# Optimization experiments

Hardware: AMD Instinct MI355X
Metric: run time of the kernel (lower is better)

Reference implementation:

```python
import jax, jax.numpy as jnp
import numpy as np

B, S, D = 2, 2048, 1024
H = 16
HD = D // H  # 64

def setup_inputs() -> dict:
    key = jax.random.key(0)
    ks = jax.random.split(key, 6)
    scale = 0.02
    return {
        "query": jax.random.normal(ks[0], (B, S, D), dtype=jnp.float32),
        "key":   jax.random.normal(ks[1], (B, S, D), dtype=jnp.float32),
        "value": jax.random.normal(ks[2], (B, S, D), dtype=jnp.float32),
        "Wq": jax.random.normal(ks[3], (D, D), dtype=jnp.float32) * scale,
        "bq": jnp.zeros((D,), dtype=jnp.float32),
        "Wk": jax.random.normal(ks[4], (D, D), dtype=jnp.float32) * scale,
        "bk": jnp.zeros((D,), dtype=jnp.float32),
        "Wv": jax.random.normal(ks[5], (D, D), dtype=jnp.float32) * scale,
        "bv": jnp.zeros((D,), dtype=jnp.float32),
    }

def reference(query, key, value, Wq, bq, Wk, bk, Wv, bv):
    b, s, d = query.shape
    # Linear projections (weights stored as (in, out))
    q = query @ Wq + bq   # [B,S,D]
    k = key   @ Wk + bk
    v = value @ Wv + bv
    # split heads -> [B,H,S,HD]
    q = q.reshape(b, s, H, HD).transpose(0, 2, 1, 3)
    k = k.reshape(b, s, H, HD).transpose(0, 2, 1, 3)
    v = v.reshape(b, s, H, HD).transpose(0, 2, 1, 3)
    # scaled dot-product attention (no mask; dropout = identity in eval)
    scores = jnp.einsum("bhqd,bhkd->bhqk", q, k) / jnp.sqrt(jnp.float32(HD))
    attn = jax.nn.softmax(scores, axis=-1)
    out = jnp.einsum("bhqk,bhkd->bhqd", attn, v)
    # merge heads -> [B,S,D]
    return out.transpose(0, 2, 1, 3).reshape(b, s, d)
```

## Files before the change

### kernel.cpp

```cpp
#include <hip/hip_runtime.h>
#include <stdint.h>

#define D_  1024
#define S_  2048
#define B_  2
#define H_  16
#define HD_ 64
#define M_  (B_*S_)
#define KVB 64

typedef unsigned short u16;
typedef __attribute__((ext_vector_type(8)))  __bf16 bf16x8;
typedef __attribute__((ext_vector_type(4)))  float  f32x4;
typedef __attribute__((ext_vector_type(16))) float  f32x16;

__device__ __forceinline__ u16 f2bf(float f) {
    __bf16 h = (__bf16)f;
    union { __bf16 h; u16 u; } x; x.h = h;
    return x.u;
}

__device__ __forceinline__ void gload_lds16(const void* g, void* l) {
    __builtin_amdgcn_global_load_lds(
        (const __attribute__((address_space(1))) uint32_t*)g,
        (__attribute__((address_space(3))) uint32_t*)l, 16, 0, 0);
}

__global__ __launch_bounds__(256) void prep_kernel(
    const float* __restrict__ q, const float* __restrict__ k, const float* __restrict__ v,
    u16* __restrict__ Xq, u16* __restrict__ Xk, u16* __restrict__ Xv,
    const float* __restrict__ Wq, const float* __restrict__ Wk, const float* __restrict__ Wv,
    u16* __restrict__ Wtq, u16* __restrict__ Wtk, u16* __restrict__ Wtv)
{
    __shared__ u16 t[64][65];
    int bid = blockIdx.x;
    if (bid < 12288) {
        int sl = bid >> 12;
        int bx = bid & 4095;
        const float* in = sl == 0 ? q : (sl == 1 ? k : v);
        u16* out = sl == 0 ? Xq : (sl == 1 ? Xk : Xv);
        int i = (bx * 256 + threadIdx.x) * 4;
        float4 vv = *(const float4*)(in + i);
        ushort4 o;
        o.x = f2bf(vv.x); o.y = f2bf(vv.y); o.z = f2bf(vv.z); o.w = f2bf(vv.w);
        *(ushort4*)(out + i) = o;
    } else {
        int tt = bid - 12288;
        int z = tt >> 8;
        int rem = tt & 255;
        const float* W = z == 0 ? Wq : (z == 1 ? Wk : Wv);
        u16* Wt = z == 0 ? Wtq : (z == 1 ? Wtk : Wtv);
        int k0 = (rem & 15) * 64, n0 = (rem >> 4) * 64;
        int tid = threadIdx.x;
        int c4 = (tid & 15) * 4, r = tid >> 4;
#pragma unroll
        for (int i = 0; i < 4; i++) {
            int row = r + i * 16;
            float4 vv = *(const float4*)(W + (uint64_t)(k0 + row) * D_ + n0 + c4);
            t[row][c4 + 0] = f2bf(vv.x);
            t[row][c4 + 1] = f2bf(vv.y);
            t[row][c4 + 2] = f2bf(vv.z);
            t[row][c4 + 3] = f2bf(vv.w);
        }
        __syncthreads();
#pragma unroll
        for (int i = 0; i < 4; i++) {
            int nrow = r + i * 16;
            ushort4 o;
            o.x = t[c4 + 0][nrow]; o.y = t[c4 + 1][nrow];
            o.z = t[c4 + 2][nrow]; o.w = t[c4 + 3][nrow];
            *(ushort4*)(Wt + (uint64_t)(n0 + nrow) * D_ + k0 + c4) = o;
        }
    }
}

__global__ __launch_bounds__(256) void gemm_qkv(
    const u16* __restrict__ Xq, const u16* __restrict__ Xk, const u16* __restrict__ Xv,
    const u16* __restrict__ Wtq, const u16* __restrict__ Wtk, const u16* __restrict__ Wtv,
    const float* __restrict__ bq, const float* __restrict__ bk, const float* __restrict__ bv,
    u16* __restrict__ Qo, u16* __restrict__ Ko, u16* __restrict__ Vo)
{
    int p = blockIdx.z;
    const u16* X    = p == 0 ? Xq  : (p == 1 ? Xk  : Xv);
    const u16* Wt   = p == 0 ? Wtq : (p == 1 ? Wtk : Wtv);
    const float* bias = p == 0 ? bq : (p == 1 ? bk : bv);
    u16* out = p == 0 ? Qo : (p == 1 ? Ko : Vo);
    float scale = p == 0 ? 0.125f : 1.0f;

    __shared__ __align__(16) u16 As[3][64 * 32];
    __shared__ __align__(16) u16 Bs[3][128 * 32];

    int tid = threadIdx.x;
    int lane = tid & 63, wid = tid >> 6;
    int lrow = lane & 15, lk = lane >> 4;
    int wr = wid >> 1, wc = wid & 1;
    int bm = blockIdx.x, bn = blockIdx.y;

    f32x4 acc[2][4] = {};

    const uint64_t Xrow0 = (uint64_t)bm * 64 * D_;
    const uint64_t Wrow0 = (uint64_t)bn * 128 * D_;

    auto stage = [&](int buf, int kt) {
        int k0 = kt * 32;
        {
            int row = tid >> 2;
            int cg = (tid & 3) ^ ((row >> 1) & 3);
            gload_lds16(X + Xrow0 + (uint64_t)row * D_ + k0 + cg * 8,
                        (char*)As[buf] + wid * 1024);
        }
#pragma unroll
        for (int it = 0; it < 2; ++it) {
            int i = it * 256 + tid;
            int row = i >> 2;
            int cg = (i & 3) ^ ((row >> 1) & 3);
            gload_lds16(Wt + Wrow0 + (uint64_t)row * D_ + k0 + cg * 8,
                        (char*)Bs[buf] + it * 4096 + wid * 1024);
        }
    };

    stage(0, 0);
    stage(1, 1);
    asm volatile("s_waitcnt vmcnt(3)" ::: "memory");
    __builtin_amdgcn_s_barrier();

    const int NKT = D_ / 32;
    for (int kt = 0; kt < NKT; ++kt) {
        int cur = kt % 3;
        if (kt + 2 < NKT) stage((kt + 2) % 3, kt + 2);

        bf16x8 a[2], b[4];
#pragma unroll
        for (int m = 0; m < 2; m++) {
            int r = wr * 32 + m * 16 + lrow;
            a[m] = *(const bf16x8*)((const char*)As[cur] + r * 64 + ((lk ^ ((r >> 1) & 3)) * 16));
        }
#pragma unroll
        for (int n = 0; n < 4; n++) {
            int r = wc * 64 + n * 16 + lrow;
            b[n] = *(const bf16x8*)((const char*)Bs[cur] + r * 64 + ((lk ^ ((r >> 1) & 3)) * 16));
        }
        if (p < 2) {
#pragma unroll
            for (int m = 0; m < 2; m++)
#pragma unroll
                for (int n = 0; n < 4; n++)
                    acc[m][n] = __builtin_amdgcn_mfma_f32_16x16x32_bf16(a[m], b[n], acc[m][n], 0, 0, 0);
        } else {
#pragma unroll
            for (int m = 0; m < 2; m++)
#pragma unroll
                for (int n = 0; n < 4; n++)
                    acc[m][n] = __builtin_amdgcn_mfma_f32_16x16x32_bf16(b[n], a[m], acc[m][n], 0, 0, 0);
        }

        if (kt + 1 < NKT) {
            if (kt + 2 < NKT)
                asm volatile("s_waitcnt vmcnt(3)" ::: "memory");
            else
                asm volatile("s_waitcnt vmcnt(0)" ::: "memory");
            __builtin_amdgcn_s_barrier();
        }
    }

    if (p < 2) {
#pragma unroll
        for (int m = 0; m < 2; m++) {
            int grow_base = bm * 64 + wr * 32 + m * 16 + lk * 4;
#pragma unroll
            for (int n = 0; n < 4; n++) {
                int gcol = bn * 128 + wc * 64 + n * 16 + lrow;
                float bb = bias[gcol];
                int h = gcol >> 6, hd = gcol & 63;
#pragma unroll
                for (int j = 0; j < 4; j++) {
                    int grow = grow_base + j;
                    int b_ = grow >> 11, s = grow & 2047;
                    out[(((uint64_t)(b_ * H_ + h)) * S_ + s) * HD_ + hd] =
                        f2bf((acc[m][n][j] + bb) * scale);
                }
            }
        }
    } else {
#pragma unroll
        for (int m = 0; m < 2; m++) {
            int sg = bm * 64 + wr * 32 + m * 16 + lrow;
            int b_ = sg >> 11, s = sg & 2047;
#pragma unroll
            for (int n = 0; n < 4; n++) {
                int ch_base = bn * 128 + wc * 64 + n * 16 + lk * 4;
#pragma unroll
                for (int j = 0; j < 4; j++) {
                    int ch = ch_base + j;
                    int h = ch >> 6, hd = ch & 63;
                    out[(((uint64_t)(b_ * H_ + h)) * HD_ + hd) * S_ + s] =
                        f2bf(acc[m][n][j] + bias[ch]);
                }
            }
        }
    }
}

__global__ __launch_bounds__(256) void attn_kernel(
    const u16* __restrict__ Q, const u16* __restrict__ K,
    const u16* __restrict__ VT, float* __restrict__ out)
{
    __shared__ __align__(16) char smem[32768];

    int lin = blockIdx.x;
    int swz = (lin & 7) * 64 + (lin >> 3);
    int qt = swz & 15, bh = swz >> 4;

    int tid = threadIdx.x;
    int w = tid >> 6, lane = tid & 63;
    int q5 = lane & 31, h = lane >> 5;

    bf16x8 qf[4];
    const u16* Qrow = Q + ((uint64_t)bh * S_ + qt * 128 + w * 32 + q5) * HD_;
#pragma unroll
    for (int kk = 0; kk < 4; kk++)
        qf[kk] = *(const bf16x8*)(Qrow + kk * 16 + h * 8);

    f32x16 o_acc[2] = {};
    float m_run = -1e30f, l_run = 0.f;

    const char* Kbase = (const char*)(K  + (uint64_t)bh * S_ * HD_);
    const char* Vbase = (const char*)(VT + (uint64_t)bh * HD_ * S_);

    auto stage = [&](int buf, int t) {
        int kv0 = t * KVB;
#pragma unroll
        for (int it = 0; it < 2; ++it) {
            int i = it * 256 + tid;
            int o = i * 16;
            int rr = o >> 7;
            int os = o ^ ((rr & 7) << 4);
            gload_lds16(Kbase + (uint64_t)kv0 * 128 + os,
                        smem + buf * 8192 + it * 4096 + w * 1024);
            gload_lds16(Vbase + (uint64_t)rr * (S_ * 2) + kv0 * 2 + (os & 127),
                        smem + 16384 + buf * 8192 + it * 4096 + w * 1024);
        }
    };

    stage(0, 0);
    __syncthreads();
    int cur = 0;

    const int NT = S_ / KVB;
    for (int t = 0; t < NT; ++t) {
        if (t + 1 < NT) stage(cur ^ 1, t + 1);

        const char* Kc = smem + cur * 8192;
        const char* Vc = smem + 16384 + cur * 8192;
        int sw = (q5 & 7) << 4;

        f32x16 sacc[2] = {};
        __builtin_amdgcn_s_setprio(1);
#pragma unroll
        for (int c = 0; c < 2; c++) {
            int rb = (c * 32 + q5) * 128;
#pragma unroll
            for (int kk = 0; kk < 4; kk++) {
                bf16x8 kf = *(const bf16x8*)(Kc + rb + ((kk * 32 + h * 16) ^ sw));
                sacc[c] = __builtin_amdgcn_mfma_f32_32x32x16_bf16(kf, qf[kk], sacc[c], 0, 0, 0);
            }
        }
        __builtin_amdgcn_s_setprio(0);

        float mp = sacc[0][0];
#pragma unroll
        for (int r = 1; r < 16; r++) mp = fmaxf(mp, sacc[0][r]);
#pragma unroll
        for (int r = 0; r < 16; r++) mp = fmaxf(mp, sacc[1][r]);
        mp = fmaxf(mp, __shfl_xor(mp, 32, 64));
        float mnew = fmaxf(m_run, mp);
        float sc = __expf(m_run - mnew);
        m_run = mnew;

        float ts = 0.f;
#pragma unroll
        for (int c = 0; c < 2; c++)
#pragma unroll
            for (int r = 0; r < 16; r++) {
                float pv = __expf(sacc[c][r] - mnew);
                sacc[c][r] = pv;
                ts += pv;
            }
        ts += __shfl_xor(ts, 32, 64);
        l_run = l_run * sc + ts;
#pragma unroll
        for (int hb = 0; hb < 2; hb++)
#pragma unroll
            for (int r = 0; r < 16; r++) o_acc[hb][r] *= sc;

        bf16x8 pa[4];
#pragma unroll
        for (int ks = 0; ks < 4; ks++) {
            int c = ks >> 1, gg = ks & 1;
            uint32_t a0, a1, b0, b1;
            asm("v_cvt_pk_bf16_f32 %0, %1, %2" : "=v"(a0) : "v"(sacc[c][8*gg+0]), "v"(sacc[c][8*gg+1]));
            asm("v_cvt_pk_bf16_f32 %0, %1, %2" : "=v"(a1) : "v"(sacc[c][8*gg+2]), "v"(sacc[c][8*gg+3]));
            asm("v_cvt_pk_bf16_f32 %0, %1, %2" : "=v"(b0) : "v"(sacc[c][8*gg+4]), "v"(sacc[c][8*gg+5]));
            asm("v_cvt_pk_bf16_f32 %0, %1, %2" : "=v"(b1) : "v"(sacc[c][8*gg+6]), "v"(sacc[c][8*gg+7]));
            asm volatile("v_permlane32_swap_b32 %0, %1" : "+v"(a0), "+v"(b0));
            asm volatile("v_permlane32_swap_b32 %0, %1" : "+v"(a1), "+v"(b1));
            union { uint32_t u[4]; bf16x8 v; } pu;
            pu.u[0] = a0; pu.u[1] = a1; pu.u[2] = b0; pu.u[3] = b1;
            pa[ks] = pu.v;
        }

        __builtin_amdgcn_s_setprio(1);
#pragma unroll
        for (int hb = 0; hb < 2; hb++) {
            int rb = (hb * 32 + q5) * 128;
#pragma unroll
            for (int ks = 0; ks < 4; ks++) {
                bf16x8 vf = *(const bf16x8*)(Vc + rb + ((ks * 32 + h * 16) ^ sw));
                o_acc[hb] = __builtin_amdgcn_mfma_f32_32x32x16_bf16(vf, pa[ks], o_acc[hb], 0, 0, 0);
            }
        }
        __builtin_amdgcn_s_setprio(0);

        __syncthreads();
        cur ^= 1;
    }

    float inv = 1.0f / l_run;
    int b_ = bh >> 4, head = bh & 15;
    int qq = lane >> 1, c0 = (lane & 1) * 16;
    float* scrw = (float*)smem + w * 1024;
    float* orow = out + ((uint64_t)(b_ * S_ + qt * 128 + w * 32 + qq)) * D_ + head * 64;
#pragma unroll
    for (int hb = 0; hb < 2; hb++) {
#pragma unroll
        for (int r = 0; r < 16; r++) {
            int col = (r & 3) + 8 * (r >> 2) + 4 * h;
            scrw[q5 * 32 + (col ^ ((q5 & 7) << 2))] = o_acc[hb][r] * inv;
        }
        __syncthreads();
#pragma unroll
        for (int j = 0; j < 4; j++) {
            int cb = c0 + j * 4;
            float4 val = *(float4*)&scrw[qq * 32 + (cb ^ ((qq & 7) << 2))];
            *(float4*)(orow + hb * 32 + cb) = val;
        }
        __syncthreads();
    }
}

extern "C" void kernel_launch(void* const* d_in, const int* in_sizes, int n_in,
                              void* d_out, int out_size, void* d_ws, size_t ws_size,
                              hipStream_t stream) {
    const float* q  = (const float*)d_in[0];
    const float* k  = (const float*)d_in[1];
    const float* v  = (const float*)d_in[2];
    const float* Wq = (const float*)d_in[3];
    const float* bq = (const float*)d_in[4];
    const float* Wk = (const float*)d_in[5];
    const float* bk = (const float*)d_in[6];
    const float* Wv = (const float*)d_in[7];
    const float* bv = (const float*)d_in[8];
    float* out = (float*)d_out;

    u16* ws = (u16*)d_ws;
    const size_t XN = (size_t)M_ * D_;
    const size_t WN = (size_t)D_ * D_;
    u16* Xq  = ws;          u16* Xk  = Xq  + XN;  u16* Xv  = Xk  + XN;
    u16* Wtq = Xv + XN;     u16* Wtk = Wtq + WN;  u16* Wtv = Wtk + WN;
    u16* Qb  = Wtv + WN;    u16* Kb  = Qb  + XN;  u16* Vb  = Kb  + XN;

    prep_kernel<<<13056, 256, 0, stream>>>(q, k, v, Xq, Xk, Xv,
                                           Wq, Wk, Wv, Wtq, Wtk, Wtv);
    gemm_qkv<<<dim3(64, 8, 3), 256, 0, stream>>>(Xq, Xk, Xv, Wtq, Wtk, Wtv,
                                                 bq, bk, bv, Qb, Kb, Vb);
    attn_kernel<<<512, 256, 0, stream>>>(Qb, Kb, Vb, out);
}
```

Measured before the change: 219.1 us.

## Use 512-thread attention blocks, exp2 softmax with lazy rescale, tree max

Folds log2(e) into the Q scale so softmax can use exp2 directly. Skips the running-max rescale of the output accumulator unless the new max exceeds the old by more than a threshold. Uses a tree reduction for the row max and split partial sums for the row sum. Attention blocks now hold 8 waves covering 256 queries, so each block does one K/V staging load per thread and the number of blocks is halved. This reduces softmax ALU work and K/V staging traffic per query, at the cost of fewer blocks (256 for 256 CUs), one block's worth of parallelism per CU, and dropping the block-order swizzle that favoured L2 reuse.

```diff
diff --git a/kernel.cpp b/kernel.cpp
--- a/kernel.cpp
+++ b/kernel.cpp
@@ -85,7 +85,7 @@
     const u16* Wt   = p == 0 ? Wtq : (p == 1 ? Wtk : Wtv);
     const float* bias = p == 0 ? bq : (p == 1 ? bk : bv);
     u16* out = p == 0 ? Qo : (p == 1 ? Ko : Vo);
-    float scale = p == 0 ? 0.125f : 1.0f;
+    float scale = p == 0 ? 0.18033688f : 1.0f;
 
     __shared__ __align__(16) u16 As[3][64 * 32];
     __shared__ __align__(16) u16 Bs[3][128 * 32];
@@ -201,22 +201,21 @@
     }
 }
 
-__global__ __launch_bounds__(256) void attn_kernel(
+__global__ __launch_bounds__(512) void attn_kernel(
     const u16* __restrict__ Q, const u16* __restrict__ K,
     const u16* __restrict__ VT, float* __restrict__ out)
 {
     __shared__ __align__(16) char smem[32768];
 
     int lin = blockIdx.x;
-    int swz = (lin & 7) * 64 + (lin >> 3);
-    int qt = swz & 15, bh = swz >> 4;
+    int bh = lin & 31, qt = lin >> 5;
 
     int tid = threadIdx.x;
     int w = tid >> 6, lane = tid & 63;
     int q5 = lane & 31, h = lane >> 5;
 
     bf16x8 qf[4];
-    const u16* Qrow = Q + ((uint64_t)bh * S_ + qt * 128 + w * 32 + q5) * HD_;
+    const u16* Qrow = Q + ((uint64_t)bh * S_ + qt * 256 + w * 32 + q5) * HD_;
 #pragma unroll
     for (int kk = 0; kk < 4; kk++)
         qf[kk] = *(const bf16x8*)(Qrow + kk * 16 + h * 8);
@@ -227,19 +226,16 @@
     const char* Kbase = (const char*)(K  + (uint64_t)bh * S_ * HD_);
     const char* Vbase = (const char*)(VT + (uint64_t)bh * HD_ * S_);
 
+    int o16 = tid * 16;
+    int rr  = o16 >> 7;
+    int os  = o16 ^ ((rr & 7) << 4);
+
     auto stage = [&](int buf, int t) {
         int kv0 = t * KVB;
-#pragma unroll
-        for (int it = 0; it < 2; ++it) {
-            int i = it * 256 + tid;
-            int o = i * 16;
-            int rr = o >> 7;
-            int os = o ^ ((rr & 7) << 4);
-            gload_lds16(Kbase + (uint64_t)kv0 * 128 + os,
-                        smem + buf * 8192 + it * 4096 + w * 1024);
-            gload_lds16(Vbase + (uint64_t)rr * (S_ * 2) + kv0 * 2 + (os & 127),
-                        smem + 16384 + buf * 8192 + it * 4096 + w * 1024);
-        }
+        gload_lds16(Kbase + (uint64_t)kv0 * 128 + os,
+                    smem + buf * 8192 + w * 1024);
+        gload_lds16(Vbase + (uint64_t)rr * (S_ * 2) + kv0 * 2 + (os & 127),
+                    smem + 16384 + buf * 8192 + w * 1024);
     };
 
     stage(0, 0);
@@ -267,31 +263,42 @@
         }
         __builtin_amdgcn_s_setprio(0);
 
-        float mp = sacc[0][0];
-#pragma unroll
-        for (int r = 1; r < 16; r++) mp = fmaxf(mp, sacc[0][r]);
-#pragma unroll
-        for (int r = 0; r < 16; r++) mp = fmaxf(mp, sacc[1][r]);
-        mp = fmaxf(mp, __shfl_xor(mp, 32, 64));
-        float mnew = fmaxf(m_run, mp);
-        float sc = __expf(m_run - mnew);
-        m_run = mnew;
-
-        float ts = 0.f;
+        float tm[16];
+#pragma unroll
+        for (int r = 0; r < 16; r++) tm[r] = fmaxf(sacc[0][r], sacc[1][r]);
+#pragma unroll
+        for (int s2 = 8; s2 > 0; s2 >>= 1)
+#pragma unroll
+            for (int r = 0; r < s2; r++) tm[r] = fmaxf(tm[r], tm[r + s2]);
+        float pmax = fmaxf(tm[0], __shfl_xor(tm[0], 32, 64));
+
+        if (!__all(pmax - m_run <= 8.0f)) {
+            float mnew = fmaxf(m_run, pmax);
+            float sc = __builtin_exp2f(m_run - mnew);
+            m_run = mnew;
+            l_run *= sc;
+#pragma unroll
+            for (int hb = 0; hb < 2; hb++)
+#pragma unroll
+                for (int r = 0; r < 16; r++) o_acc[hb][r] *= sc;
+        }
+
+        float ts0 = 0.f, ts1 = 0.f, ts2 = 0.f, ts3 = 0.f;
 #pragma unroll
         for (int c = 0; c < 2; c++)
 #pragma unroll
-            for (int r = 0; r < 16; r++) {
-                float pv = __expf(sacc[c][r] - mnew);
-                sacc[c][r] = pv;
-                ts += pv;
-            }
+            for (int r = 0; r < 16; r += 4) {
+                float p0 = __builtin_exp2f(sacc[c][r + 0] - m_run);
+                float p1 = __builtin_exp2f(sacc[c][r + 1] - m_run);
+                float p2 = __builtin_exp2f(sacc[c][r + 2] - m_run);
+                float p3 = __builtin_exp2f(sacc[c][r + 3] - m_run);
+                sacc[c][r + 0] = p0; sacc[c][r + 1] = p1;
+                sacc[c][r + 2] = p2; sacc[c][r + 3] = p3;
+                ts0 += p0; ts1 += p1; ts2 += p2; ts3 += p3;
+            }
+        float ts = (ts0 + ts1) + (ts2 + ts3);
         ts += __shfl_xor(ts, 32, 64);
-        l_run = l_run * sc + ts;
-#pragma unroll
-        for (int hb = 0; hb < 2; hb++)
-#pragma unroll
-            for (int r = 0; r < 16; r++) o_acc[hb][r] *= sc;
+        l_run += ts;
 
         bf16x8 pa[4];
 #pragma unroll
@@ -329,7 +336,7 @@
     int b_ = bh >> 4, head = bh & 15;
     int qq = lane >> 1, c0 = (lane & 1) * 16;
     float* scrw = (float*)smem + w * 1024;
-    float* orow = out + ((uint64_t)(b_ * S_ + qt * 128 + w * 32 + qq)) * D_ + head * 64;
+    float* orow = out + ((uint64_t)(b_ * S_ + qt * 256 + w * 32 + qq)) * D_ + head * 64;
 #pragma unroll
     for (int hb = 0; hb < 2; hb++) {
 #pragma unroll
@@ -373,5 +380,5 @@
                                            Wq, Wk, Wv, Wtq, Wtk, Wtv);
     gemm_qkv<<<dim3(64, 8, 3), 256, 0, stream>>>(Xq, Xk, Xv, Wtq, Wtk, Wtv,
                                                  bq, bk, bv, Qb, Kb, Vb);
-    attn_kernel<<<512, 256, 0, stream>>>(Qb, Kb, Vb, out);
-}
+    attn_kernel<<<256, 512, 0, stream>>>(Qb, Kb, Vb, out);
+}
```

Result: slower. 224.0 us (+2.2%).
